# Kernel optimization log

Measured on AMD Instinct MI355X. Metric: run time of the kernel, lower is better.

## Reference

```python
import jax, jax.numpy as jnp
import numpy as np

NUM_NODES = 10101   # 1 root + 100 supers + 10000 leaves
NUM_LEAVES = 10000
TEMPERATURE = 1.0
# weights from the source: root_weight=0, super_weight=1, leaf_weight=1
PATH_WEIGHTS = np.array([0.0, 1.0, 1.0], dtype=np.float32)
TOTAL_WEIGHT = float(PATH_WEIGHTS.sum())


def setup_inputs() -> dict:
    key = jax.random.key(0)
    k1, k2 = jax.random.split(key)
    features = jax.random.normal(k1, (8192, 128), dtype=jnp.float32)
    prototypes = jax.random.normal(k2, (NUM_NODES, 128), dtype=jnp.float32)
    # hierarchy: leaf i (node id 101+i) -> path [root=0, super=1+i//100, leaf=101+i]
    leaf = np.arange(NUM_LEAVES)
    path_idx = np.stack([np.zeros(NUM_LEAVES, dtype=np.int32),
                         (1 + leaf // 100).astype(np.int32),
                         (101 + leaf).astype(np.int32)], axis=1)  # [L, 3]
    return {"features": features, "prototypes": prototypes,
            "path_idx": jnp.asarray(path_idx)}


def reference(features, prototypes, path_idx):
    # ProCoLoss stand-in: node-level logits [N, num_nodes]
    node_logits = jnp.einsum('nd,cd->nc', features, prototypes) / TEMPERATURE
    # gather 3 path logits per leaf and weighted-sum (replaces per-leaf loop)
    gathered = node_logits[:, path_idx]                      # [N, L, 3]
    w = jnp.asarray(PATH_WEIGHTS)
    leaf_logits = jnp.einsum('nlk,k->nl', gathered, w) / TOTAL_WEIGHT  # [N, L]
    return leaf_logits
```

## Files before the change

### kernel.cpp

```cpp
#include <hip/hip_runtime.h>
#include <hip/hip_bf16.h>
#include <stdint.h>

#define M_DIM      8192
#define K_DIM      128
#define NUM_LEAVES 10000
#define N_PAD      10112
#define NT         79
#define MT         64
#define LDS_STRIDE 136

typedef __attribute__((ext_vector_type(8))) short bf16x8;
typedef __attribute__((ext_vector_type(4))) float f32x4;

static __device__ __forceinline__ unsigned short f2bf(float f) {
    union { float f; uint32_t u; } v; v.f = f;
    uint32_t u = v.u;
    u += 0x7FFFu + ((u >> 16) & 1u);
    return (unsigned short)(u >> 16);
}

__global__ void prep_features(const float* __restrict__ F, unsigned short* __restrict__ Fb) {
    int t = blockIdx.x * blockDim.x + threadIdx.x;
    float4 v = ((const float4*)F)[t];
    ushort4 o;
    o.x = f2bf(v.x); o.y = f2bf(v.y); o.z = f2bf(v.z); o.w = f2bf(v.w);
    ((ushort4*)Fb)[t] = o;
}

__global__ void prep_q(const float* __restrict__ P, const int* __restrict__ idx,
                       unsigned short* __restrict__ Qb) {
    int t = blockIdx.x * blockDim.x + threadIdx.x;
    int l = t >> 5;
    int c = (t & 31) << 2;
    ushort4 o;
    if (l < NUM_LEAVES) {
        int i1 = idx[l * 3 + 1];
        int i2 = idx[l * 3 + 2];
        float4 a = *(const float4*)&P[(size_t)i1 * K_DIM + c];
        float4 b = *(const float4*)&P[(size_t)i2 * K_DIM + c];
        o.x = f2bf(0.5f * (a.x + b.x));
        o.y = f2bf(0.5f * (a.y + b.y));
        o.z = f2bf(0.5f * (a.z + b.z));
        o.w = f2bf(0.5f * (a.w + b.w));
    } else {
        o.x = 0; o.y = 0; o.z = 0; o.w = 0;
    }
    *(ushort4*)&Qb[(size_t)l * K_DIM + c] = o;
}

__global__ __launch_bounds__(256, 2) void gemm_fq(
    const unsigned short* __restrict__ Fb,
    const unsigned short* __restrict__ Qb,
    float* __restrict__ out) {
    __shared__ unsigned short As[128 * LDS_STRIDE];
    __shared__ unsigned short Bs[128 * LDS_STRIDE];

    const int bn = blockIdx.x;
    const int bm = blockIdx.y;
    const int tid = threadIdx.x;

    {
        const uint4* gA = (const uint4*)(Fb + (size_t)bm * 128 * K_DIM);
        const uint4* gB = (const uint4*)(Qb + (size_t)bn * 128 * K_DIM);
#pragma unroll
        for (int i = 0; i < 8; ++i) {
            int c = tid + i * 256;
            int r = c >> 4;
            int c8 = (c & 15) << 3;
            uint4 va = gA[c];
            uint4 vb = gB[c];
            *(uint4*)&As[r * LDS_STRIDE + c8] = va;
            *(uint4*)&Bs[r * LDS_STRIDE + c8] = vb;
        }
    }
    __syncthreads();

    const int lane = tid & 63;
    const int w    = tid >> 6;
    const int wm   = (w >> 1) * 64;
    const int wn   = (w & 1) * 64;
    const int l15  = lane & 15;
    const int quad = lane >> 4;

    f32x4 acc[4][4] = {};

#pragma unroll
    for (int kt = 0; kt < 4; ++kt) {
        const int k0 = kt * 32 + quad * 8;
        bf16x8 af[4], bfr[4];
#pragma unroll
        for (int i = 0; i < 4; ++i) {
            af[i]  = *(const bf16x8*)&As[(wm + i * 16 + l15) * LDS_STRIDE + k0];
            bfr[i] = *(const bf16x8*)&Bs[(wn + i * 16 + l15) * LDS_STRIDE + k0];
        }
#pragma unroll
        for (int mi = 0; mi < 4; ++mi)
#pragma unroll
            for (int ni = 0; ni < 4; ++ni)
                acc[mi][ni] = __builtin_amdgcn_mfma_f32_16x16x32_bf16(
                    bfr[ni], af[mi], acc[mi][ni], 0, 0, 0);
    }

    const int nbase = bm * 128 + wm + l15;
    const int cbase = bn * 128 + wn + quad * 4;
#pragma unroll
    for (int mi = 0; mi < 4; ++mi) {
        float* rowp = out + (size_t)(nbase + mi * 16) * NUM_LEAVES;
#pragma unroll
        for (int ni = 0; ni < 4; ++ni) {
            int c = cbase + ni * 16;
            if (c < NUM_LEAVES) {
                __builtin_nontemporal_store(acc[mi][ni], (f32x4*)(rowp + c));
            }
        }
    }
}

extern "C" void kernel_launch(void* const* d_in, const int* in_sizes, int n_in,
                              void* d_out, int out_size, void* d_ws, size_t ws_size,
                              hipStream_t stream) {
    const float* F  = (const float*)d_in[0];
    const float* P  = (const float*)d_in[1];
    const int* idx  = (const int*)d_in[2];
    float* out      = (float*)d_out;

    unsigned short* Fb = (unsigned short*)d_ws;
    unsigned short* Qb = Fb + (size_t)M_DIM * K_DIM;

    prep_features<<<(M_DIM * K_DIM / 4) / 256, 256, 0, stream>>>(F, Fb);
    prep_q<<<(N_PAD * 32) / 256, 256, 0, stream>>>(P, idx, Qb);
    gemm_fq<<<dim3(NT, MT), 256, 0, stream>>>(Fb, Qb, out);
}
```

Measured before the change: 366.3 us.

## Restructure GEMM into row-strip blocks streaming Q tiles with LDS-transposed stores

Replaces the 2D 128x128 tiled GEMM with a 1D grid where each block owns 16 feature rows held in registers and walks all 79 column tiles. Q fragments are loaded straight from global memory into registers with double buffering, and no LDS staging is used for inputs. Results are transposed through a small XOR-swizzled LDS buffer so each row is written as contiguous float4 segments, and the nontemporal hint is dropped. The kernel is bound by writing the 327MB output, so the aim is more coalesced, streaming stores and higher occupancy, at the cost of rereading Q from L2 in every block.

```diff
diff --git a/kernel.cpp b/kernel.cpp
--- a/kernel.cpp
+++ b/kernel.cpp
@@ -6,9 +6,8 @@
 #define K_DIM      128
 #define NUM_LEAVES 10000
 #define N_PAD      10112
-#define NT         79
-#define MT         64
-#define LDS_STRIDE 136
+#define TILES      79
+#define ROWS_PB    16
 
 typedef __attribute__((ext_vector_type(8))) short bf16x8;
 typedef __attribute__((ext_vector_type(4))) float f32x4;
@@ -49,72 +48,83 @@
     *(ushort4*)&Qb[(size_t)l * K_DIM + c] = o;
 }
 
-__global__ __launch_bounds__(256, 2) void gemm_fq(
+__device__ __forceinline__ void tile_step(
+    const bf16x8 (&bq)[8], const bf16x8 (&a4)[4],
+    float* __restrict__ Tw, float* __restrict__ out,
+    int t, int R0, int wn, int l15, int quad, int lane)
+{
+    f32x4 acc[2] = {};
+#pragma unroll
+    for (int kt = 0; kt < 4; ++kt) {
+#pragma unroll
+        for (int ni = 0; ni < 2; ++ni)
+            acc[ni] = __builtin_amdgcn_mfma_f32_16x16x32_bf16(
+                bq[ni * 4 + kt], a4[kt], acc[ni], 0, 0, 0);
+    }
+#pragma unroll
+    for (int ni = 0; ni < 2; ++ni) {
+        int chunk = (ni * 4 + quad) ^ (l15 & 7);
+        *(f32x4*)&Tw[l15 * 32 + chunk * 4] = acc[ni];
+    }
+    const int h3 = lane >> 3;
+    const int c8 = lane & 7;
+    const int rchunk = c8 ^ h3;
+    const int c = t * 128 + wn + c8 * 4;
+#pragma unroll
+    for (int it = 0; it < 2; ++it) {
+        int r = it * 8 + h3;
+        f32x4 v = *(const f32x4*)&Tw[r * 32 + rchunk * 4];
+        if (c < NUM_LEAVES) {
+            *(f32x4*)&out[(size_t)(R0 + r) * NUM_LEAVES + c] = v;
+        }
+    }
+}
+
+#define LOADB(dst, t)                                                              \
+    do {                                                                           \
+        _Pragma("unroll")                                                          \
+        for (int ni = 0; ni < 2; ++ni) {                                           \
+            _Pragma("unroll")                                                      \
+            for (int kt = 0; kt < 4; ++kt)                                         \
+                dst[ni * 4 + kt] = *(const bf16x8*)&qbase[(size_t)(t) * 16384 +    \
+                                                          ni * 2048 + kt * 32];    \
+        }                                                                          \
+    } while (0)
+
+__global__ __launch_bounds__(256, 4) void gemm_rows(
     const unsigned short* __restrict__ Fb,
     const unsigned short* __restrict__ Qb,
-    float* __restrict__ out) {
-    __shared__ unsigned short As[128 * LDS_STRIDE];
-    __shared__ unsigned short Bs[128 * LDS_STRIDE];
+    float* __restrict__ out)
+{
+    __shared__ float T[4][16 * 32];
 
-    const int bn = blockIdx.x;
-    const int bm = blockIdx.y;
-    const int tid = threadIdx.x;
-
-    {
-        const uint4* gA = (const uint4*)(Fb + (size_t)bm * 128 * K_DIM);
-        const uint4* gB = (const uint4*)(Qb + (size_t)bn * 128 * K_DIM);
-#pragma unroll
-        for (int i = 0; i < 8; ++i) {
-            int c = tid + i * 256;
-            int r = c >> 4;
-            int c8 = (c & 15) << 3;
-            uint4 va = gA[c];
-            uint4 vb = gB[c];
-            *(uint4*)&As[r * LDS_STRIDE + c8] = va;
-            *(uint4*)&Bs[r * LDS_STRIDE + c8] = vb;
-        }
-    }
-    __syncthreads();
-
+    const int tid  = threadIdx.x;
     const int lane = tid & 63;
     const int w    = tid >> 6;
-    const int wm   = (w >> 1) * 64;
-    const int wn   = (w & 1) * 64;
     const int l15  = lane & 15;
     const int quad = lane >> 4;
+    const int wn   = w * 32;
+    const int R0   = blockIdx.x * ROWS_PB;
+    float* Tw = &T[w][0];
 
-    f32x4 acc[4][4] = {};
+    bf16x8 a4[4];
+#pragma unroll
+    for (int kt = 0; kt < 4; ++kt)
+        a4[kt] = *(const bf16x8*)&Fb[(size_t)(R0 + l15) * K_DIM + kt * 32 + quad * 8];
 
-#pragma unroll
-    for (int kt = 0; kt < 4; ++kt) {
-        const int k0 = kt * 32 + quad * 8;
-        bf16x8 af[4], bfr[4];
-#pragma unroll
-        for (int i = 0; i < 4; ++i) {
-            af[i]  = *(const bf16x8*)&As[(wm + i * 16 + l15) * LDS_STRIDE + k0];
-            bfr[i] = *(const bf16x8*)&Bs[(wn + i * 16 + l15) * LDS_STRIDE + k0];
-        }
-#pragma unroll
-        for (int mi = 0; mi < 4; ++mi)
-#pragma unroll
-            for (int ni = 0; ni < 4; ++ni)
-                acc[mi][ni] = __builtin_amdgcn_mfma_f32_16x16x32_bf16(
-                    bfr[ni], af[mi], acc[mi][ni], 0, 0, 0);
+    const unsigned short* qbase = Qb + (size_t)(wn + l15) * K_DIM + quad * 8;
+
+    bf16x8 bA[8], bB[8];
+    LOADB(bA, 0);
+#pragma unroll 1
+    for (int it = 0; it < 39; ++it) {
+        const int t0 = it * 2;
+        LOADB(bB, t0 + 1);
+        tile_step(bA, a4, Tw, out, t0, R0, wn, l15, quad, lane);
+        LOADB(bA, t0 + 2);
+        tile_step(bB, a4, Tw, out, t0 + 1, R0, wn, l15, quad, lane);
     }
-
-    const int nbase = bm * 128 + wm + l15;
-    const int cbase = bn * 128 + wn + quad * 4;
-#pragma unroll
-    for (int mi = 0; mi < 4; ++mi) {
-        float* rowp = out + (size_t)(nbase + mi * 16) * NUM_LEAVES;
-#pragma unroll
-        for (int ni = 0; ni < 4; ++ni) {
-            int c = cbase + ni * 16;
-            if (c < NUM_LEAVES) {
-                __builtin_nontemporal_store(acc[mi][ni], (f32x4*)(rowp + c));
-            }
-        }
-    }
+    tile_step(bA, a4, Tw, out, 78, R0, wn, l15, quad, lane);
 }
 
 extern "C" void kernel_launch(void* const* d_in, const int* in_sizes, int n_in,
@@ -130,5 +140,5 @@
 
     prep_features<<<(M_DIM * K_DIM / 4) / 256, 256, 0, stream>>>(F, Fb);
     prep_q<<<(N_PAD * 32) / 256, 256, 0, stream>>>(P, idx, Qb);
-    gemm_fq<<<dim3(NT, MT), 256, 0, stream>>>(Fb, Qb, out);
+    gemm_rows<<<M_DIM / ROWS_PB, 256, 0, stream>>>(Fb, Qb, out);
 }
```

New measurement: 450.0 us. 1.23x slower.
